# Performance work log

Measured on AMD Instinct MI355X. Metric: run time of the kernel, lower is better.

Reference implementation:

```python
import jax, jax.numpy as jnp
import numpy as np

# Model config (mirrors Mamba2Block(dim=256) with mamba_ssm defaults)
D_MODEL = 256
EXPAND = 2
D_INNER = D_MODEL * EXPAND          # 512
HEADDIM = D_MODEL * EXPAND // 8     # 64
NHEADS = D_INNER // HEADDIM         # 8
D_STATE = 64
D_CONV = 4
CONV_DIM = D_INNER + 2 * D_STATE    # 640 (ngroups=1)
D_IN_PROJ = 2 * D_INNER + 2 * D_STATE + NHEADS  # 1160
BATCH, SEQLEN = 2, 2048
EPS = 1e-5


def setup_inputs() -> dict:
    key = jax.random.key(0)
    ks = jax.random.split(key, 12)
    s = 0.02
    return {
        "hidden_states": jax.random.normal(ks[0], (BATCH, SEQLEN, D_MODEL), jnp.float32),
        "norm_w": jnp.ones((D_MODEL,), jnp.float32),
        "norm_b": jnp.zeros((D_MODEL,), jnp.float32),
        "W_in": jax.random.normal(ks[1], (D_MODEL, D_IN_PROJ), jnp.float32) * s,
        "conv_w": jax.random.normal(ks[2], (CONV_DIM, D_CONV), jnp.float32) * 0.25,
        "conv_b": jnp.zeros((CONV_DIM,), jnp.float32),
        "dt_bias": jax.random.uniform(ks[3], (NHEADS,), jnp.float32),
        "A_log": jax.random.uniform(ks[4], (NHEADS,), jnp.float32),  # A = -exp(A_log) in (-e, -1]
        "D_param": jnp.ones((NHEADS,), jnp.float32),
        "rms_w": jnp.ones((D_INNER,), jnp.float32),
        "W_out": jax.random.normal(ks[5], (D_INNER, D_MODEL), jnp.float32) * s,
    }


def _layer_norm(x, w, b):
    mu = jnp.mean(x, -1, keepdims=True)
    var = jnp.mean((x - mu) ** 2, -1, keepdims=True)
    return (x - mu) * jax.lax.rsqrt(var + EPS) * w + b


def _causal_depthwise_conv(x, w, b):
    # x: [B,L,C], w: [C,K] depthwise causal conv
    B, L, C = x.shape
    K = w.shape[1]
    xp = jnp.pad(x, ((0, 0), (K - 1, 0), (0, 0)))
    y = b
    for k in range(K):  # K=4, fixed small kernel
        y = y + w[:, k] * xp[:, k:k + L, :]
    return y


def reference(hidden_states, norm_w, norm_b, W_in, conv_w, conv_b, dt_bias, A_log, D_param, rms_w, W_out):
    B, L, D = hidden_states.shape
    residual = hidden_states                       # residual is None, drop_path=0
    x = _layer_norm(residual, norm_w, norm_b)      # pre-norm

    zxbcdt = jnp.einsum("bld,de->ble", x, W_in)    # [B,L,2*Di+2*N+H]
    z = zxbcdt[..., :D_INNER]
    xBC = zxbcdt[..., D_INNER:D_INNER + CONV_DIM]
    dt = zxbcdt[..., -NHEADS:]

    xBC = jax.nn.silu(_causal_depthwise_conv(xBC, conv_w, conv_b))
    xs = xBC[..., :D_INNER]
    Bm = xBC[..., D_INNER:D_INNER + D_STATE]       # [B,L,N] (ngroups=1)
    Cm = xBC[..., D_INNER + D_STATE:]              # [B,L,N]

    dt = jax.nn.softplus(dt + dt_bias)             # [B,L,H]
    A = -jnp.exp(A_log)                            # [H]
    dA = jnp.exp(dt * A)                           # [B,L,H]

    xh = xs.reshape(B, L, NHEADS, HEADDIM)         # [B,L,H,P]
    dtx = dt[..., None] * xh                       # [B,L,H,P]

    def step(s, inp):
        dA_t, dtx_t, B_t, C_t = inp                # [B,H],[B,H,P],[B,N],[B,N]
        s = s * dA_t[:, :, None, None] + dtx_t[..., None] * B_t[:, None, None, :]
        y_t = jnp.einsum("bhpn,bn->bhp", s, C_t)
        return s, y_t

    s0 = jnp.zeros((B, NHEADS, HEADDIM, D_STATE), hidden_states.dtype)
    xs_in = (jnp.swapaxes(dA, 0, 1), jnp.swapaxes(dtx, 0, 1),
             jnp.swapaxes(Bm, 0, 1), jnp.swapaxes(Cm, 0, 1))
    _, ys = jax.lax.scan(step, s0, xs_in)          # ys: [L,B,H,P]
    y = jnp.swapaxes(ys, 0, 1) + D_param[None, None, :, None] * xh  # skip term
    y = y.reshape(B, L, D_INNER)

    # gated RMSNorm (norm_before_gate=False): rmsnorm(y * silu(z)) * rms_w
    g = y * jax.nn.silu(z)
    g = g * jax.lax.rsqrt(jnp.mean(g * g, -1, keepdims=True) + EPS) * rms_w

    out = jnp.einsum("bld,de->ble", g, W_out)
    return out, residual
```

## Files before the change

### kernel.cpp

```cpp
#include <hip/hip_runtime.h>
#include <hip/hip_bf16.h>

#define BATCH 2
#define SEQLEN 2048
#define DMODEL 256
#define DINNER 512
#define NHEADS 8
#define HEADDIM 64
#define DSTATE 64
#define CONVDIM 640
#define DINPROJ 1160
#define NTOK (BATCH*SEQLEN)
#define Q 64
#define NCH (SEQLEN/Q)
#define NPAD2 1280
#define TS 72
#define RS3 196
#define GS 536

typedef short v8s __attribute__((ext_vector_type(8)));
typedef float v4f __attribute__((ext_vector_type(4)));

__device__ __forceinline__ unsigned short f2bf(float f){
    __hip_bfloat16 h = __float2bfloat16(f);
    return *reinterpret_cast<unsigned short*>(&h);
}
__device__ __forceinline__ float bf2f(unsigned short u){
    unsigned int x = ((unsigned int)u) << 16;
    return __uint_as_float(x);
}
__device__ __forceinline__ void gload_lds16(const unsigned short* g, unsigned short* l){
    __builtin_amdgcn_global_load_lds((const __attribute__((address_space(1))) void*)g,
                                     (__attribute__((address_space(3))) void*)l, 16, 0, 0);
}

__global__ __launch_bounds__(256) void k_prep(
        const float* __restrict__ hid, const float* __restrict__ nw, const float* __restrict__ nb,
        const float* __restrict__ Win, const float* __restrict__ Wout, const float* __restrict__ rms_w,
        float* __restrict__ res, unsigned short* __restrict__ Xb,
        unsigned short* __restrict__ Wti, unsigned short* __restrict__ Wto){
    int bx = blockIdx.x;
    int t = threadIdx.x;
    if(bx < 256){
        __shared__ float xs[16][DMODEL];
        int tok0 = bx*16;
        for(int i=0;i<16;i++){
            int idx = i*256+t; int j = idx>>8, c = idx&255;
            float v = hid[(size_t)(tok0+j)*DMODEL + c];
            xs[j][c] = v;
            res[(size_t)(tok0+j)*DMODEL + c] = v;
        }
        __syncthreads();
        int g = t>>4, il = t&15;
        float sum=0.f, sumsq=0.f;
        for(int i=0;i<16;i++){ float v = xs[g][il*16+i]; sum += v; sumsq += v*v; }
        #pragma unroll
        for(int m=1;m<16;m<<=1){ sum += __shfl_xor(sum,m); sumsq += __shfl_xor(sumsq,m); }
        float mu   = sum*(1.f/256.f);
        float var  = sumsq*(1.f/256.f) - mu*mu;
        float rstd = rsqrtf(var + 1e-5f);
        for(int i=0;i<16;i++){
            int c = il*16+i;
            xs[g][c] = (xs[g][c]-mu)*rstd*nw[c] + nb[c];
        }
        __syncthreads();
        for(int i=0;i<16;i++){
            int idx = i*256+t; int j = idx>>8, c = idx&255;
            Xb[(size_t)(tok0+j)*DMODEL + c] = f2bf(xs[j][c]);
        }
    } else if(bx < 256 + NPAD2/4){
        int n0 = (bx-256)*4, k = t;
        #pragma unroll
        for(int i=0;i<4;i++){
            int n = n0+i;
            float v = (n < DINPROJ) ? Win[(size_t)k*DINPROJ + n] : 0.f;
            Wti[(size_t)n*DMODEL + k] = f2bf(v);
        }
    } else {
        int n0 = (bx - 256 - NPAD2/4)*4;
        #pragma unroll
        for(int kk=0;kk<2;kk++){
            int k = t + kk*256;
            float rw = rms_w[k];
            #pragma unroll
            for(int i=0;i<4;i++){
                int n = n0+i;
                Wto[(size_t)n*DINNER + k] = f2bf(Wout[(size_t)k*DMODEL + n] * rw);
            }
        }
    }
}

__global__ __launch_bounds__(256) void k_gemm_in(
        const unsigned short* __restrict__ A, const unsigned short* __restrict__ Bt,
        unsigned short* __restrict__ zxb){
    __shared__ __align__(16) unsigned short As[64*256];
    __shared__ __align__(16) unsigned short Bs[64*256];
    int t = threadIdx.x;
    int lane = t & 63, w = t >> 6;
    int lanelow = lane & 15, quad = lane >> 4;
    int tok0 = blockIdx.x * 64;
    int n0   = blockIdx.y * 64;
    int rw = (w & 1) * 32, cw = (w >> 1) * 32;
    #pragma unroll
    for(int k=0;k<8;k++){
        int u = t + k*256;
        int row = u >> 5, off = u & 31;
        int soff = off ^ (row & 7);
        gload_lds16(A  + (size_t)(tok0+row)*DMODEL + soff*8, &As[(w*64 + k*256)*8]);
        gload_lds16(Bt + (size_t)(n0 +row)*DMODEL + soff*8, &Bs[(w*64 + k*256)*8]);
    }
    __syncthreads();
    v4f acc[2][2];
    #pragma unroll
    for(int mi=0;mi<2;mi++)
        #pragma unroll
        for(int ni=0;ni<2;ni++)
            acc[mi][ni] = (v4f){0.f,0.f,0.f,0.f};
    #pragma unroll
    for(int k0=0;k0<8;k0++){
        v8s a[2], b[2];
        #pragma unroll
        for(int mi=0;mi<2;mi++){
            int r = rw + mi*16 + lanelow;
            a[mi] = *(const v8s*)&As[r*256 + (((k0*4 + quad) ^ (r & 7)))*8];
        }
        #pragma unroll
        for(int ni=0;ni<2;ni++){
            int r = cw + ni*16 + lanelow;
            b[ni] = *(const v8s*)&Bs[r*256 + (((k0*4 + quad) ^ (r & 7)))*8];
        }
        #pragma unroll
        for(int mi=0;mi<2;mi++)
            #pragma unroll
            for(int ni=0;ni<2;ni++)
                acc[mi][ni] = __builtin_amdgcn_mfma_f32_16x16x32_bf16(a[mi], b[ni], acc[mi][ni], 0,0,0);
    }
    #pragma unroll
    for(int mi=0;mi<2;mi++){
        #pragma unroll
        for(int ni=0;ni<2;ni++){
            int col = n0 + cw + ni*16 + lanelow;
            if(col < DINPROJ){
                #pragma unroll
                for(int r=0;r<4;r++){
                    int row = tok0 + rw + mi*16 + quad*4 + r;
                    zxb[(size_t)row*DINPROJ + col] = f2bf(acc[mi][ni][r]);
                }
            }
        }
    }
}

__global__ __launch_bounds__(256) void k_chunk1(
        const unsigned short* __restrict__ zxb, const float* __restrict__ conv_w, const float* __restrict__ conv_b,
        const float* __restrict__ dt_bias, const float* __restrict__ A_log, const float* __restrict__ D_param,
        unsigned short* __restrict__ yw16, unsigned short* __restrict__ contrib16,
        float* __restrict__ Larr, float* __restrict__ decayArr, unsigned short* __restrict__ Ccv){
    int blk = blockIdx.x;
    int c = blk & 31, h = (blk>>5)&7, b = blk>>8;
    int t = threadIdx.x;
    int lane = t & 63, w = t >> 6;
    int lanelow = lane & 15, quad = lane >> 4;
    __shared__ __align__(16) unsigned short Cb[64*TS];
    __shared__ __align__(16) unsigned short Bb[64*TS];
    __shared__ __align__(16) unsigned short BtW[64*TS];
    __shared__ __align__(16) unsigned short Xt[64*TS];
    __shared__ __align__(16) unsigned short BufRegion[2*19*RS3];
    __shared__ float Ls[Q], dts[Q], wch[Q];
    unsigned short* Gbuf = BufRegion;
    int l0 = c*Q;
    int bh = b*NHEADS + h;
    const unsigned short* zbase = zxb + (size_t)(b*SEQLEN + l0)*DINPROJ;

    {
        unsigned short* buf = BufRegion;
        #pragma unroll
        for(int i=0;i<4;i++){
            int u = t + 256*i;
            if(u < 19*48){
                int row = u/48, seg = u - row*48;
                int l = l0 - 3 + row;
                int gcol = (seg<16) ? (DINNER + h*HEADDIM + seg*4) : (2*DINNER + (seg-16)*4);
                ushort4 v;
                if(l >= 0) v = *(const ushort4*)(zxb + ((size_t)b*SEQLEN + l)*DINPROJ + gcol);
                else { v.x=0; v.y=0; v.z=0; v.w=0; }
                *(ushort4*)&buf[row*RS3 + seg*4] = v;
            }
        }
    }
    if(t < Q){
        float v = bf2f(zbase[(size_t)t*DINPROJ + (DINPROJ-NHEADS) + h]) + dt_bias[h];
        float dt = (v > 20.f) ? v : log1pf(__expf(v));
        float A  = -__expf(A_log[h]);
        float ld = dt*A;
        #pragma unroll
        for(int off=1; off<64; off<<=1){
            float u = __shfl_up(ld, off);
            if(lane >= off) ld += u;
        }
        Ls[t] = ld; dts[t] = dt;
        float l63 = __shfl(ld, 63);
        wch[t] = __expf(l63 - ld) * dt;
    }
    __syncthreads();

    unsigned short* CcP = Ccv + ((size_t)b*NCH + c)*4096;
    for(int s=0; s<4; s++){
        unsigned short* cur = BufRegion + (s&1)*(19*RS3);
        unsigned short* nxt = BufRegion + ((s+1)&1)*(19*RS3);
        ushort4 stg[4];
        if(s < 3){
            #pragma unroll
            for(int i=0;i<4;i++){
                int u = t + 256*i;
                if(u < 19*48){
                    int row = u/48, seg = u - row*48;
                    int l = l0 + (s+1)*16 - 3 + row;
                    int gcol = (seg<16) ? (DINNER + h*HEADDIM + seg*4) : (2*DINNER + (seg-16)*4);
                    stg[i] = *(const ushort4*)(zxb + ((size_t)b*SEQLEN + l)*DINPROJ + gcol);
                }
            }
        }
        #pragma unroll
        for(int i=0;i<3;i++){
            int u = t + 256*i;
            int stl = u & 15, grp = u >> 4;
            int st = s*16 + stl;
            int ch = grp*4;
            float xk[4][4];
            #pragma unroll
            for(int k=0;k<4;k++){
                ushort4 v = *(const ushort4*)&cur[(stl+k)*RS3 + ch];
                xk[k][0]=bf2f(v.x); xk[k][1]=bf2f(v.y); xk[k][2]=bf2f(v.z); xk[k][3]=bf2f(v.w);
            }
            float wst = wch[st];
            #pragma unroll
            for(int j=0;j<4;j++){
                int chj = ch+j;
                int cc = (chj<64) ? (h*HEADDIM + chj) : (448 + chj);
                float4 wv = *(const float4*)&conv_w[cc*4];
                float acc = conv_b[cc] + wv.x*xk[0][j] + wv.y*xk[1][j] + wv.z*xk[2][j] + wv.w*xk[3][j];
                float sv = acc/(1.f+__expf(-acc));
                if(chj < 64){
                    Xt[chj*TS + st] = f2bf(sv);
                } else if(chj < 128){
                    int n = chj-64;
                    Bb[st*TS + n]  = f2bf(sv);
                    BtW[n*TS + st] = f2bf(sv*wst);
                } else {
                    int n = chj-128;
                    unsigned short sb16 = f2bf(sv);
                    Cb[st*TS + n] = sb16;
                    if(h==0) CcP[st*64 + n] = sb16;
                }
            }
        }
        if(s < 3){
            #pragma unroll
            for(int i=0;i<4;i++){
                int u = t + 256*i;
                if(u < 19*48){
                    int row = u/48, seg = u - row*48;
                    *(ushort4*)&nxt[row*RS3 + seg*4] = stg[i];
                }
            }
        }
        __syncthreads();
    }
    v4f g[4];
    #pragma unroll
    for(int nt=0;nt<4;nt++) g[nt] = (v4f){0.f,0.f,0.f,0.f};
    #pragma unroll
    for(int kk=0;kk<2;kk++){
        v8s a = *(const v8s*)&Cb[(w*16+lanelow)*TS + kk*32 + quad*8];
        #pragma unroll
        for(int nt=0;nt<4;nt++){
            v8s bb = *(const v8s*)&Bb[(nt*16+lanelow)*TS + kk*32 + quad*8];
            g[nt] = __builtin_amdgcn_mfma_f32_16x16x32_bf16(a, bb, g[nt], 0,0,0);
        }
    }
    float Lrow[4];
    #pragma unroll
    for(int r=0;r<4;r++) Lrow[r] = Ls[w*16 + quad*4 + r];
    #pragma unroll
    for(int nt=0;nt<4;nt++){
        int col = nt*16 + lanelow;
        float Lc = Ls[col], dtc = dts[col];
        #pragma unroll
        for(int r=0;r<4;r++){
            int rowg = w*16 + quad*4 + r;
            float val = (col <= rowg) ? g[nt][r] * __expf(Lrow[r]-Lc) * dtc : 0.f;
            Gbuf[rowg*TS + col] = f2bf(val);
        }
    }
    __syncthreads();
    v4f ya[4], sa[4];
    #pragma unroll
    for(int nt=0;nt<4;nt++){ ya[nt]=(v4f){0.f,0.f,0.f,0.f}; sa[nt]=(v4f){0.f,0.f,0.f,0.f}; }
    #pragma unroll
    for(int kk=0;kk<2;kk++){
        v8s ag = *(const v8s*)&Gbuf[(w*16+lanelow)*TS + kk*32 + quad*8];
        v8s ax = *(const v8s*)&Xt[(w*16+lanelow)*TS + kk*32 + quad*8];
        #pragma unroll
        for(int nt=0;nt<4;nt++){
            v8s bx = *(const v8s*)&Xt[(nt*16+lanelow)*TS + kk*32 + quad*8];
            v8s bw = *(const v8s*)&BtW[(nt*16+lanelow)*TS + kk*32 + quad*8];
            ya[nt] = __builtin_amdgcn_mfma_f32_16x16x32_bf16(ag, bx, ya[nt], 0,0,0);
            sa[nt] = __builtin_amdgcn_mfma_f32_16x16x32_bf16(ax, bw, sa[nt], 0,0,0);
        }
    }
    float Dp = D_param[h];
    #pragma unroll
    for(int nt=0;nt<4;nt++){
        int col = nt*16 + lanelow;
        #pragma unroll
        for(int r=0;r<4;r++){
            int i = w*16 + quad*4 + r;
            float xval = bf2f(Xt[col*TS + i]);
            yw16[((size_t)b*SEQLEN + l0 + i)*DINNER + h*HEADDIM + col] = f2bf(ya[nt][r] + Dp*xval);
            contrib16[(((size_t)bh*NCH + c)*64 + i)*64 + col] = f2bf(sa[nt][r]);
        }
    }
    if(t < Q) Larr[((size_t)bh*NCH + c)*Q + t] = Ls[t];
    if(t == 0) decayArr[bh*NCH + c] = __expf(Ls[Q-1]);
}

__global__ __launch_bounds__(256) void k_chunk2(const unsigned short* __restrict__ contrib16,
                                                const float* __restrict__ decayArr,
                                                unsigned short* __restrict__ Sb){
    int bh = blockIdx.x >> 4;
    int part = blockIdx.x & 15;
    int e = part*256 + threadIdx.x;
    const size_t base = (size_t)bh*NCH*4096 + e;
    float vals[NCH];
    #pragma unroll
    for(int c=0;c<NCH;c++) vals[c] = bf2f(contrib16[base + (size_t)c*4096]);
    float s = 0.f;
    #pragma unroll
    for(int c=0;c<NCH;c++){
        Sb[base + (size_t)c*4096] = f2bf(s);
        s = fmaf(s, decayArr[bh*NCH + c], vals[c]);
    }
}

__global__ __launch_bounds__(512) void k_tail(
        const unsigned short* __restrict__ Ccv, const unsigned short* __restrict__ Sb,
        const float* __restrict__ Larr, const unsigned short* __restrict__ yw16,
        const unsigned short* __restrict__ zxb, const unsigned short* __restrict__ Wto,
        float* __restrict__ out){
    int blk = blockIdx.x;
    int q4 = blk & 3, c = (blk>>2) & 31, b = blk >> 7;
    int t = threadIdx.x;
    int h = t >> 6, lane = t & 63;
    int lanelow = lane & 15, quad = lane >> 4;
    int bh = b*NHEADS + h;
    __shared__ __align__(16) unsigned short Gs[16*GS];
    __shared__ float wsum[8][16];
    __shared__ float rstdS[16];
    const unsigned short* Cp = Ccv + ((size_t)b*NCH + c)*4096;
    const unsigned short* Sp = Sb + ((size_t)bh*NCH + c)*4096;
    int row0 = q4*16;
    v8s a0 = *(const v8s*)(Cp + (row0+lanelow)*64 + quad*8);
    v8s a1 = *(const v8s*)(Cp + (row0+lanelow)*64 + 32 + quad*8);
    v8s s[4][2];
    #pragma unroll
    for(int nt=0;nt<4;nt++){
        s[nt][0] = *(const v8s*)(Sp + (nt*16+lanelow)*64 + quad*8);
        s[nt][1] = *(const v8s*)(Sp + (nt*16+lanelow)*64 + 32 + quad*8);
    }
    float sq[4] = {0.f,0.f,0.f,0.f};
    const float* Lp = Larr + ((size_t)bh*NCH + c)*Q;
    float eL[4];
    #pragma unroll
    for(int r=0;r<4;r++) eL[r] = __expf(Lp[row0 + quad*4 + r]);
    size_t tok0 = (size_t)b*SEQLEN + c*Q + row0;
    #pragma unroll
    for(int nt=0;nt<4;nt++){
        v4f acc = (v4f){0.f,0.f,0.f,0.f};
        acc = __builtin_amdgcn_mfma_f32_16x16x32_bf16(a0, s[nt][0], acc, 0,0,0);
        acc = __builtin_amdgcn_mfma_f32_16x16x32_bf16(a1, s[nt][1], acc, 0,0,0);
        int col = h*HEADDIM + nt*16 + lanelow;
        #pragma unroll
        for(int r=0;r<4;r++){
            size_t tok = tok0 + quad*4 + r;
            float yv = acc[r]*eL[r] + bf2f(yw16[tok*DINNER + col]);
            float z  = bf2f(zxb[tok*DINPROJ + col]);
            float gg = yv * (z/(1.f+__expf(-z)));
            Gs[(quad*4+r)*GS + col] = f2bf(gg);
            sq[r] += gg*gg;
        }
    }
    #pragma unroll
    for(int r=0;r<4;r++){
        float v = sq[r];
        #pragma unroll
        for(int m=1;m<16;m<<=1) v += __shfl_xor(v, m);
        sq[r] = v;
    }
    if(lanelow==0){
        #pragma unroll
        for(int r=0;r<4;r++) wsum[h][quad*4 + r] = sq[r];
    }
    __syncthreads();
    if(t < 16){
        float tot = 0.f;
        #pragma unroll
        for(int hh=0;hh<8;hh++) tot += wsum[hh][t];
        rstdS[t] = rsqrtf(tot*(1.f/512.f) + 1e-5f);
    }
    __syncthreads();
    v4f acc2[2];
    #pragma unroll
    for(int nt=0;nt<2;nt++) acc2[nt] = (v4f){0.f,0.f,0.f,0.f};
    for(int ki=0; ki<16; ki++){
        v8s a = *(const v8s*)&Gs[lanelow*GS + ki*32 + quad*8];
        #pragma unroll
        for(int nt=0;nt<2;nt++){
            v8s bfr = *(const v8s*)(Wto + (size_t)(h*32 + nt*16 + lanelow)*DINNER + ki*32 + quad*8);
            acc2[nt] = __builtin_amdgcn_mfma_f32_16x16x32_bf16(a, bfr, acc2[nt], 0,0,0);
        }
    }
    float rs[4];
    #pragma unroll
    for(int r=0;r<4;r++) rs[r] = rstdS[quad*4 + r];
    #pragma unroll
    for(int nt=0;nt<2;nt++){
        int col = h*32 + nt*16 + lanelow;
        #pragma unroll
        for(int r=0;r<4;r++)
            out[(tok0 + quad*4 + r)*DMODEL + col] = acc2[nt][r]*rs[r];
    }
}

extern "C" void kernel_launch(void* const* d_in, const int* in_sizes, int n_in,
                              void* d_out, int out_size, void* d_ws, size_t ws_size,
                              hipStream_t stream) {
    const float* hid     = (const float*)d_in[0];
    const float* norm_w  = (const float*)d_in[1];
    const float* norm_b  = (const float*)d_in[2];
    const float* Win     = (const float*)d_in[3];
    const float* conv_w  = (const float*)d_in[4];
    const float* conv_b  = (const float*)d_in[5];
    const float* dt_bias = (const float*)d_in[6];
    const float* A_log   = (const float*)d_in[7];
    const float* D_param = (const float*)d_in[8];
    const float* rms_w   = (const float*)d_in[9];
    const float* Wout    = (const float*)d_in[10];

    unsigned short* contrib16 = (unsigned short*)d_ws;
    float* Larr    = (float*)(contrib16 + (size_t)16*NCH*4096);
    float* decayA  = Larr + (size_t)16*NCH*Q;
    unsigned short* zxb  = (unsigned short*)(decayA + 512);
    unsigned short* yw16 = zxb + (size_t)NTOK*DINPROJ;
    unsigned short* Sb   = yw16 + (size_t)NTOK*DINNER;
    unsigned short* Ccv  = Sb + (size_t)16*NCH*4096;
    unsigned short* Xb   = Ccv + (size_t)BATCH*NCH*4096;
    unsigned short* Wti  = Xb + (size_t)NTOK*DMODEL;
    unsigned short* Wto  = Wti + (size_t)NPAD2*DMODEL;

    float* out = (float*)d_out;
    float* res = out + (size_t)NTOK*DMODEL;

    k_prep<<<256 + NPAD2/4 + DMODEL/4, 256, 0, stream>>>(hid, norm_w, norm_b, Win, Wout, rms_w, res, Xb, Wti, Wto);
    k_gemm_in<<<dim3(NTOK/64, NPAD2/64), 256, 0, stream>>>(Xb, Wti, zxb);
    k_chunk1<<<BATCH*NHEADS*NCH, 256, 0, stream>>>(zxb, conv_w, conv_b, dt_bias, A_log, D_param,
                                                   yw16, contrib16, Larr, decayA, Ccv);
    k_chunk2<<<256, 256, 0, stream>>>(contrib16, decayA, Sb);
    k_tail<<<BATCH*NCH*4, 512, 0, stream>>>(Ccv, Sb, Larr, yw16, zxb, Wto, out);
}
```

Baseline: 123.8 us.

## Fuse layernorm and weight conversion into input GEMM; merge chunk scan into tail via grid barrier

New measurement: 246.1 us. +98.8%, slower.

```diff
diff --git a/kernel.cpp b/kernel.cpp
--- a/kernel.cpp
+++ b/kernel.cpp
@@ -13,7 +13,6 @@
 #define NTOK (BATCH*SEQLEN)
 #define Q 64
 #define NCH (SEQLEN/Q)
-#define NPAD2 1280
 #define TS 72
 #define RS3 196
 #define GS 536
@@ -29,88 +28,86 @@
     unsigned int x = ((unsigned int)u) << 16;
     return __uint_as_float(x);
 }
-__device__ __forceinline__ void gload_lds16(const unsigned short* g, unsigned short* l){
-    __builtin_amdgcn_global_load_lds((const __attribute__((address_space(1))) void*)g,
-                                     (__attribute__((address_space(3))) void*)l, 16, 0, 0);
-}
-
-__global__ __launch_bounds__(256) void k_prep(
+
+__global__ __launch_bounds__(256) void k_fused_in(
         const float* __restrict__ hid, const float* __restrict__ nw, const float* __restrict__ nb,
         const float* __restrict__ Win, const float* __restrict__ Wout, const float* __restrict__ rms_w,
-        float* __restrict__ res, unsigned short* __restrict__ Xb,
-        unsigned short* __restrict__ Wti, unsigned short* __restrict__ Wto){
-    int bx = blockIdx.x;
+        float* __restrict__ res, unsigned short* __restrict__ zxb, unsigned short* __restrict__ Wto){
+    int bx = blockIdx.x, by = blockIdx.y;
     int t = threadIdx.x;
-    if(bx < 256){
-        __shared__ float xs[16][DMODEL];
-        int tok0 = bx*16;
+    int tok0 = bx*64;
+    if(by == 19){
+        #pragma unroll
         for(int i=0;i<16;i++){
-            int idx = i*256+t; int j = idx>>8, c = idx&255;
-            float v = hid[(size_t)(tok0+j)*DMODEL + c];
-            xs[j][c] = v;
-            res[(size_t)(tok0+j)*DMODEL + c] = v;
-        }
-        __syncthreads();
-        int g = t>>4, il = t&15;
-        float sum=0.f, sumsq=0.f;
-        for(int i=0;i<16;i++){ float v = xs[g][il*16+i]; sum += v; sumsq += v*v; }
-        #pragma unroll
-        for(int m=1;m<16;m<<=1){ sum += __shfl_xor(sum,m); sumsq += __shfl_xor(sumsq,m); }
-        float mu   = sum*(1.f/256.f);
-        float var  = sumsq*(1.f/256.f) - mu*mu;
-        float rstd = rsqrtf(var + 1e-5f);
-        for(int i=0;i<16;i++){
-            int c = il*16+i;
-            xs[g][c] = (xs[g][c]-mu)*rstd*nw[c] + nb[c];
-        }
-        __syncthreads();
-        for(int i=0;i<16;i++){
-            int idx = i*256+t; int j = idx>>8, c = idx&255;
-            Xb[(size_t)(tok0+j)*DMODEL + c] = f2bf(xs[j][c]);
-        }
-    } else if(bx < 256 + NPAD2/4){
-        int n0 = (bx-256)*4, k = t;
-        #pragma unroll
-        for(int i=0;i<4;i++){
-            int n = n0+i;
-            float v = (n < DINPROJ) ? Win[(size_t)k*DINPROJ + n] : 0.f;
-            Wti[(size_t)n*DMODEL + k] = f2bf(v);
-        }
-    } else {
-        int n0 = (bx - 256 - NPAD2/4)*4;
-        #pragma unroll
-        for(int kk=0;kk<2;kk++){
-            int k = t + kk*256;
-            float rw = rms_w[k];
-            #pragma unroll
-            for(int i=0;i<4;i++){
-                int n = n0+i;
-                Wto[(size_t)n*DINNER + k] = f2bf(Wout[(size_t)k*DMODEL + n] * rw);
-            }
-        }
-    }
-}
-
-__global__ __launch_bounds__(256) void k_gemm_in(
-        const unsigned short* __restrict__ A, const unsigned short* __restrict__ Bt,
-        unsigned short* __restrict__ zxb){
+            int u = t + i*256;
+            int row = u>>6, c4 = u&63;
+            float4 v = *(const float4*)(hid + (size_t)(tok0+row)*DMODEL + c4*4);
+            *(float4*)(res + (size_t)(tok0+row)*DMODEL + c4*4) = v;
+        }
+        int n  = bx*4 + (t>>6);
+        int k0 = (t&63)*8;
+        union { v8s v; unsigned short u[8]; } pk;
+        #pragma unroll
+        for(int m=0;m<8;m++){
+            int k = k0+m;
+            pk.u[m] = f2bf(Wout[(size_t)k*DMODEL + n] * rms_w[k]);
+        }
+        *(v8s*)&Wto[(size_t)n*DINNER + k0] = pk.v;
+        return;
+    }
     __shared__ __align__(16) unsigned short As[64*256];
     __shared__ __align__(16) unsigned short Bs[64*256];
-    int t = threadIdx.x;
+    int n0 = by*64;
+    {
+        int j = t>>2, p = t&3;
+        const float* hp = hid + (size_t)(tok0+j)*DMODEL + p*64;
+        float xv[64];
+        float sum=0.f, sq=0.f;
+        #pragma unroll
+        for(int i=0;i<16;i++){
+            float4 v = *(const float4*)(hp + i*4);
+            xv[i*4+0]=v.x; xv[i*4+1]=v.y; xv[i*4+2]=v.z; xv[i*4+3]=v.w;
+            sum += v.x+v.y+v.z+v.w;
+            sq  += v.x*v.x + v.y*v.y + v.z*v.z + v.w*v.w;
+        }
+        sum += __shfl_xor(sum,1); sq += __shfl_xor(sq,1);
+        sum += __shfl_xor(sum,2); sq += __shfl_xor(sq,2);
+        float mu   = sum*(1.f/256.f);
+        float var  = sq*(1.f/256.f) - mu*mu;
+        float rstd = rsqrtf(var + 1e-5f);
+        #pragma unroll
+        for(int i=0;i<8;i++){
+            union { v8s v; unsigned short u[8]; } pk;
+            #pragma unroll
+            for(int m=0;m<8;m++){
+                int c  = i*8+m;
+                int ch = p*64 + c;
+                pk.u[m] = f2bf((xv[c]-mu)*rstd*nw[ch] + nb[ch]);
+            }
+            int chunk = p*8 + i;
+            *(v8s*)&As[j*256 + ((chunk ^ (j&7)))*8] = pk.v;
+        }
+    }
+    {
+        int n_l = t&63, g = t>>6;
+        int nglob = n0 + n_l;
+        #pragma unroll
+        for(int i=0;i<8;i++){
+            int chunk = g*8 + i;
+            union { v8s v; unsigned short u[8]; } pk;
+            #pragma unroll
+            for(int m=0;m<8;m++){
+                int k = chunk*8 + m;
+                float v = (nglob < DINPROJ) ? Win[(size_t)k*DINPROJ + nglob] : 0.f;
+                pk.u[m] = f2bf(v);
+            }
+            *(v8s*)&Bs[n_l*256 + ((chunk ^ (n_l&7)))*8] = pk.v;
+        }
+    }
+    __syncthreads();
     int lane = t & 63, w = t >> 6;
     int lanelow = lane & 15, quad = lane >> 4;
-    int tok0 = blockIdx.x * 64;
-    int n0   = blockIdx.y * 64;
     int rw = (w & 1) * 32, cw = (w >> 1) * 32;
-    #pragma unroll
-    for(int k=0;k<8;k++){
-        int u = t + k*256;
-        int row = u >> 5, off = u & 31;
-        int soff = off ^ (row & 7);
-        gload_lds16(A  + (size_t)(tok0+row)*DMODEL + soff*8, &As[(w*64 + k*256)*8]);
-        gload_lds16(Bt + (size_t)(n0 +row)*DMODEL + soff*8, &Bs[(w*64 + k*256)*8]);
-    }
-    __syncthreads();
     v4f acc[2][2];
     #pragma unroll
     for(int mi=0;mi<2;mi++)
@@ -156,12 +153,14 @@
         const unsigned short* __restrict__ zxb, const float* __restrict__ conv_w, const float* __restrict__ conv_b,
         const float* __restrict__ dt_bias, const float* __restrict__ A_log, const float* __restrict__ D_param,
         unsigned short* __restrict__ yw16, unsigned short* __restrict__ contrib16,
-        float* __restrict__ Larr, float* __restrict__ decayArr, unsigned short* __restrict__ Ccv){
+        float* __restrict__ Larr, float* __restrict__ decayArr, unsigned short* __restrict__ Ccv,
+        unsigned int* __restrict__ bar){
     int blk = blockIdx.x;
     int c = blk & 31, h = (blk>>5)&7, b = blk>>8;
     int t = threadIdx.x;
     int lane = t & 63, w = t >> 6;
     int lanelow = lane & 15, quad = lane >> 4;
+    if(blk==0 && t==0) *bar = 0u;
     __shared__ __align__(16) unsigned short Cb[64*TS];
     __shared__ __align__(16) unsigned short Bb[64*TS];
     __shared__ __align__(16) unsigned short BtW[64*TS];
@@ -326,32 +325,36 @@
     if(t == 0) decayArr[bh*NCH + c] = __expf(Ls[Q-1]);
 }
 
-__global__ __launch_bounds__(256) void k_chunk2(const unsigned short* __restrict__ contrib16,
-                                                const float* __restrict__ decayArr,
-                                                unsigned short* __restrict__ Sb){
-    int bh = blockIdx.x >> 4;
-    int part = blockIdx.x & 15;
-    int e = part*256 + threadIdx.x;
-    const size_t base = (size_t)bh*NCH*4096 + e;
-    float vals[NCH];
-    #pragma unroll
-    for(int c=0;c<NCH;c++) vals[c] = bf2f(contrib16[base + (size_t)c*4096]);
-    float s = 0.f;
-    #pragma unroll
-    for(int c=0;c<NCH;c++){
-        Sb[base + (size_t)c*4096] = f2bf(s);
-        s = fmaf(s, decayArr[bh*NCH + c], vals[c]);
-    }
-}
-
-__global__ __launch_bounds__(512) void k_tail(
-        const unsigned short* __restrict__ Ccv, const unsigned short* __restrict__ Sb,
+__global__ __launch_bounds__(512) void k_tail2(
+        const unsigned short* __restrict__ Ccv, unsigned short* __restrict__ Sb,
         const float* __restrict__ Larr, const unsigned short* __restrict__ yw16,
         const unsigned short* __restrict__ zxb, const unsigned short* __restrict__ Wto,
-        float* __restrict__ out){
+        const unsigned short* __restrict__ contrib16, const float* __restrict__ decayA,
+        unsigned int* __restrict__ bar, float* __restrict__ out){
     int blk = blockIdx.x;
+    int t = threadIdx.x;
+    if(t < 256){
+        int bh2 = blk>>4, part = blk&15;
+        size_t base = (size_t)bh2*NCH*4096 + part*256 + t;
+        float vals[NCH];
+        #pragma unroll
+        for(int c2=0;c2<NCH;c2++) vals[c2] = bf2f(contrib16[base + (size_t)c2*4096]);
+        float s0 = 0.f;
+        #pragma unroll
+        for(int c2=0;c2<NCH;c2++){
+            Sb[base + (size_t)c2*4096] = f2bf(s0);
+            s0 = fmaf(s0, decayA[bh2*NCH + c2], vals[c2]);
+        }
+    }
+    __threadfence();
+    __syncthreads();
+    if(t == 0){
+        atomicAdd(bar, 1u);
+        while(atomicAdd(bar, 0u) < 256u){ __builtin_amdgcn_s_sleep(8); }
+        __threadfence();
+    }
+    __syncthreads();
     int q4 = blk & 3, c = (blk>>2) & 31, b = blk >> 7;
-    int t = threadIdx.x;
     int h = t >> 6, lane = t & 63;
     int lanelow = lane & 15, quad = lane >> 4;
     int bh = b*NHEADS + h;
@@ -451,21 +454,18 @@
     unsigned short* contrib16 = (unsigned short*)d_ws;
     float* Larr    = (float*)(contrib16 + (size_t)16*NCH*4096);
     float* decayA  = Larr + (size_t)16*NCH*Q;
-    unsigned short* zxb  = (unsigned short*)(decayA + 512);
+    unsigned int* bar = (unsigned int*)(decayA + 512);
+    unsigned short* zxb  = (unsigned short*)(bar + 16);
     unsigned short* yw16 = zxb + (size_t)NTOK*DINPROJ;
     unsigned short* Sb   = yw16 + (size_t)NTOK*DINNER;
     unsigned short* Ccv  = Sb + (size_t)16*NCH*4096;
-    unsigned short* Xb   = Ccv + (size_t)BATCH*NCH*4096;
-    unsigned short* Wti  = Xb + (size_t)NTOK*DMODEL;
-    unsigned short* Wto  = Wti + (size_t)NPAD2*DMODEL;
+    unsigned short* Wto  = Ccv + (size_t)BATCH*NCH*4096;
 
     float* out = (float*)d_out;
     float* res = out + (size_t)NTOK*DMODEL;
 
-    k_prep<<<256 + NPAD2/4 + DMODEL/4, 256, 0, stream>>>(hid, norm_w, norm_b, Win, Wout, rms_w, res, Xb, Wti, Wto);
-    k_gemm_in<<<dim3(NTOK/64, NPAD2/64), 256, 0, stream>>>(Xb, Wti, zxb);
+    k_fused_in<<<dim3(NTOK/64, 20), 256, 0, stream>>>(hid, norm_w, norm_b, Win, Wout, rms_w, res, zxb, Wto);
     k_chunk1<<<BATCH*NHEADS*NCH, 256, 0, stream>>>(zxb, conv_w, conv_b, dt_bias, A_log, D_param,
-                                                   yw16, contrib16, Larr, decayA, Ccv);
-    k_chunk2<<<256, 256, 0, stream>>>(contrib16, decayA, Sb);
-    k_tail<<<BATCH*NCH*4, 512, 0, stream>>>(Ccv, Sb, Larr, yw16, zxb, Wto, out);
-}
+                                                   yw16, contrib16, Larr, decayA, Ccv, bar);
+    k_tail2<<<BATCH*NCH*4, 512, 0, stream>>>(Ccv, Sb, Larr, yw16, zxb, Wto, contrib16, decayA, bar, out);
+}
```
